# Kernel tuning notes

Hardware: AMD Instinct MI355X
Metric: run time of the kernel (lower is better)

Reference implementation:

```python
import jax, jax.numpy as jnp
import numpy as np

N_LAGS = 64
UNBIASED = False


def setup_inputs() -> dict:
    key = jax.random.key(0)
    X = jax.random.normal(key, (4096, 8192), dtype=jnp.float32)
    return {"X": X}


def reference(X) -> jnp.ndarray:
    # X: [B, T]
    B, T = X.shape
    Xc = X - jnp.mean(X, axis=1, keepdims=True)  # center per sequence
    acs = []
    for k in range(N_LAGS + 1):  # small fixed loop over lags
        denom = (T - k) if UNBIASED else T
        # sum_{t} Xc[b, t] * Xc[b, t+k]
        ac_k = jnp.einsum('bt,bt->b', Xc[:, : T - k], Xc[:, k:]) / denom
        acs.append(ac_k)
    Xautocorr = jnp.stack(acs, axis=1)  # [B, n_lags+1]
    # normalize lags 1..n_lags by lag-0 variance
    return Xautocorr[:, 1:] / Xautocorr[:, :1]
```

## Files before the change

### kernel.cpp

```cpp
#include <hip/hip_runtime.h>


typedef __bf16 bf16x8 __attribute__((ext_vector_type(8)));
typedef float f32x16 __attribute__((ext_vector_type(16)));
typedef unsigned int uint32;

#define T_LEN 8192
#define XT_STRIDE 264
#define XT_SHORTS (32 * XT_STRIDE)
#define WPB 3

__device__ __forceinline__ short f2bf(float f) {
  uint32 u = __builtin_bit_cast(uint32, f);
  return (short)((u + 0x7fffu + ((u >> 16) & 1u)) >> 16);
}

__global__ __launch_bounds__(WPB * 64, 1)
void autocorr_kernel(const float* __restrict__ X, float* __restrict__ out, int nrows) {
  __shared__ short xt_all[WPB * XT_SHORTS];
  const int wave = threadIdx.x >> 6;
  const int lane = threadIdx.x & 63;
  const int row = blockIdx.x * WPB + wave;
  if (row >= nrows) return;
  short* xt = xt_all + wave * XT_SHORTS;

  {
    int rr = lane >> 1;
    int off = 256 + ((lane & 1) << 2);
    *(int2*)(xt + rr * XT_STRIDE + off) = make_int2(0, 0);
  }

  const float4* __restrict__ Xv = (const float4*)(X + (size_t)row * T_LEN);
  float ssum = 0.f;
#pragma unroll 8
  for (int rr = 0; rr < 32; ++rr) {
    float4 v = Xv[(rr << 6) + lane];
    ssum += (v.x + v.y) + (v.z + v.w);
    int t0 = (rr << 8) + (lane << 2);
    int b = (t0 & 31) * XT_STRIDE + (t0 >> 5);
    xt[b]                 = f2bf(v.x);
    xt[b + XT_STRIDE]     = f2bf(v.y);
    xt[b + 2 * XT_STRIDE] = f2bf(v.z);
    xt[b + 3 * XT_STRIDE] = f2bf(v.w);
  }
  for (int d = 32; d > 0; d >>= 1) ssum += __shfl_xor(ssum, d, 64);

  const int r = lane & 31;
  const int hi = lane >> 5;
  f32x16 g0 = {}, g1 = {}, g2 = {};
  const short* xr = xt + r * XT_STRIDE + (hi << 3);
#pragma unroll 4
  for (int c = 0; c < 16; ++c) {
    const short* p = xr + (c << 4);
    int4 a4 = *(const int4*)p;
    int e89 = *(const int*)(p + 8);
    uint32 u0 = a4.x, u1 = a4.y, u2 = a4.z, u3 = a4.w, u4 = (uint32)e89;
    int4 b1;
    b1.x = (u0 >> 16) | (u1 << 16);
    b1.y = (u1 >> 16) | (u2 << 16);
    b1.z = (u2 >> 16) | (u3 << 16);
    b1.w = (u3 >> 16) | (u4 << 16);
    int4 b2;
    b2.x = u1; b2.y = u2; b2.z = u3; b2.w = u4;
    bf16x8 fa = __builtin_bit_cast(bf16x8, a4);
    bf16x8 f1 = __builtin_bit_cast(bf16x8, b1);
    bf16x8 f2 = __builtin_bit_cast(bf16x8, b2);
    g0 = __builtin_amdgcn_mfma_f32_32x32x16_bf16(fa, fa, g0, 0, 0, 0);
    g1 = __builtin_amdgcn_mfma_f32_32x32x16_bf16(fa, f1, g1, 0, 0, 0);
    g2 = __builtin_amdgcn_mfma_f32_32x32x16_bf16(fa, f2, g2, 0, 0, 0);
  }

  float* gbuf = (float*)xt;
#pragma unroll
  for (int v = 0; v < 16; ++v) {
    int rm = (v & 3) + (hi << 2) + ((v >> 2) << 3);
    gbuf[(rm)      * 33 + r] = g0[v];
    gbuf[(32 + rm) * 33 + r] = g1[v];
    gbuf[(64 + rm) * 33 + r] = g2[v];
  }

  int k = lane + 1;
  int s = k & 31, q = k >> 5;
  float ck = 0.f;
#pragma unroll 4
  for (int m = 0; m < 32; ++m) {
    int ms = m + s;
    int dd = q + (ms >> 5);
    ck += gbuf[(dd * 32 + m) * 33 + (ms & 31)];
  }
  float c0 = 0.f;
#pragma unroll 4
  for (int m = 0; m < 32; ++m) c0 += gbuf[m * 33 + m];

  float P = X[(size_t)row * T_LEN + lane];
  float Q = X[(size_t)row * T_LEN + (T_LEN - 1 - lane)];
  for (int d = 1; d < 64; d <<= 1) {
    float tp = __shfl_up(P, (unsigned)d, 64);
    float tq = __shfl_up(Q, (unsigned)d, 64);
    if (lane >= d) { P += tp; Q += tq; }
  }
  float mu = ssum * (1.0f / (float)T_LEN);
  float Ck = ck - mu * (2.f * ssum - P - Q) + (float)(T_LEN - k) * mu * mu;
  float C0 = c0 - mu * 2.f * ssum + (float)T_LEN * mu * mu;
  out[(size_t)row * 64 + lane] = Ck / C0;
}

extern "C" void kernel_launch(void* const* d_in, const int* in_sizes, int n_in,
                              void* d_out, int out_size, void* d_ws, size_t ws_size,
                              hipStream_t stream) {
  const float* X = (const float*)d_in[0];
  float* out = (float*)d_out;
  int nrows = in_sizes[0] / T_LEN;
  dim3 grid((nrows + WPB - 1) / WPB);
  autocorr_kernel<<<grid, dim3(WPB * 64), 0, stream>>>(X, out, nrows);
}
```

Baseline: 192.6 us.

## Feed MFMA operands directly from global loads and shrink LDS for occupancy

```diff
diff --git a/kernel.cpp b/kernel.cpp
--- a/kernel.cpp
+++ b/kernel.cpp
@@ -6,91 +6,100 @@
 typedef unsigned int uint32;
 
 #define T_LEN 8192
-#define XT_STRIDE 264
-#define XT_SHORTS (32 * XT_STRIDE)
-#define WPB 3
+#define WPB 4
+#define GB_STRIDE 34
+#define GB_SHORTS (96 * GB_STRIDE)
 
+__device__ __forceinline__ uint32 pack2bf(float a, float b) {
+  uint32 ua = __builtin_bit_cast(uint32, a);
+  uint32 ub = __builtin_bit_cast(uint32, b);
+  ua += 0x7fffu + ((ua >> 16) & 1u);
+  ub += 0x7fffu + ((ub >> 16) & 1u);
+  return (ua >> 16) | (ub & 0xffff0000u);
+}
 __device__ __forceinline__ short f2bf(float f) {
   uint32 u = __builtin_bit_cast(uint32, f);
   return (short)((u + 0x7fffu + ((u >> 16) & 1u)) >> 16);
 }
+__device__ __forceinline__ float bf2f(short h) {
+  uint32 u = ((uint32)(unsigned short)h) << 16;
+  return __builtin_bit_cast(float, u);
+}
 
-__global__ __launch_bounds__(WPB * 64, 1)
+__global__ __launch_bounds__(WPB * 64, 4)
 void autocorr_kernel(const float* __restrict__ X, float* __restrict__ out, int nrows) {
-  __shared__ short xt_all[WPB * XT_SHORTS];
+  __shared__ short gb_all[WPB * GB_SHORTS];
   const int wave = threadIdx.x >> 6;
   const int lane = threadIdx.x & 63;
   const int row = blockIdx.x * WPB + wave;
   if (row >= nrows) return;
-  short* xt = xt_all + wave * XT_SHORTS;
+  short* gb = gb_all + wave * GB_SHORTS;
 
-  {
-    int rr = lane >> 1;
-    int off = 256 + ((lane & 1) << 2);
-    *(int2*)(xt + rr * XT_STRIDE + off) = make_int2(0, 0);
+  const int m = lane & 31;
+  const int sh = lane >> 5;
+  const float* __restrict__ base = X + (size_t)row * T_LEN + (sh << 8) + m;
+
+  f32x16 g0 = {}, g1 = {}, g2 = {};
+  float ssum = 0.f;
+
+#define CHUNK_BODY(PP, E8, E9)                                                  \
+  {                                                                             \
+    float e0 = (PP)[0],   e1 = (PP)[32],  e2 = (PP)[64],  e3 = (PP)[96];        \
+    float e4 = (PP)[128], e5 = (PP)[160], e6 = (PP)[192], e7 = (PP)[224];       \
+    float e8 = (E8), e9 = (E9);                                                 \
+    ssum += ((e0 + e1) + (e2 + e3)) + ((e4 + e5) + (e6 + e7));                  \
+    uint32 u0 = pack2bf(e0, e1), u1 = pack2bf(e2, e3), u2 = pack2bf(e4, e5);    \
+    uint32 u3 = pack2bf(e6, e7), u4 = pack2bf(e8, e9);                          \
+    int4 a4 = make_int4((int)u0, (int)u1, (int)u2, (int)u3);                    \
+    int4 b1;                                                                    \
+    b1.x = (int)((u0 >> 16) | (u1 << 16));                                      \
+    b1.y = (int)((u1 >> 16) | (u2 << 16));                                      \
+    b1.z = (int)((u2 >> 16) | (u3 << 16));                                      \
+    b1.w = (int)((u3 >> 16) | (u4 << 16));                                      \
+    int4 b2 = make_int4((int)u1, (int)u2, (int)u3, (int)u4);                    \
+    bf16x8 fa = __builtin_bit_cast(bf16x8, a4);                                 \
+    bf16x8 f1 = __builtin_bit_cast(bf16x8, b1);                                 \
+    bf16x8 f2 = __builtin_bit_cast(bf16x8, b2);                                 \
+    g0 = __builtin_amdgcn_mfma_f32_32x32x16_bf16(fa, fa, g0, 0, 0, 0);          \
+    g1 = __builtin_amdgcn_mfma_f32_32x32x16_bf16(fa, f1, g1, 0, 0, 0);          \
+    g2 = __builtin_amdgcn_mfma_f32_32x32x16_bf16(fa, f2, g2, 0, 0, 0);          \
   }
 
-  const float4* __restrict__ Xv = (const float4*)(X + (size_t)row * T_LEN);
-  float ssum = 0.f;
-#pragma unroll 8
-  for (int rr = 0; rr < 32; ++rr) {
-    float4 v = Xv[(rr << 6) + lane];
-    ssum += (v.x + v.y) + (v.z + v.w);
-    int t0 = (rr << 8) + (lane << 2);
-    int b = (t0 & 31) * XT_STRIDE + (t0 >> 5);
-    xt[b]                 = f2bf(v.x);
-    xt[b + XT_STRIDE]     = f2bf(v.y);
-    xt[b + 2 * XT_STRIDE] = f2bf(v.z);
-    xt[b + 3 * XT_STRIDE] = f2bf(v.w);
+#pragma unroll 3
+  for (int c = 0; c < 15; ++c) {
+    const float* p = base + (c << 9);
+    CHUNK_BODY(p, p[256], p[288])
   }
+  {
+    const float* p = base + (15 << 9);
+    float e8s = 0.f, e9s = 0.f;
+    if (!sh) { e8s = p[256]; e9s = p[288]; }
+    CHUNK_BODY(p, e8s, e9s)
+  }
+#undef CHUNK_BODY
+
   for (int d = 32; d > 0; d >>= 1) ssum += __shfl_xor(ssum, d, 64);
 
-  const int r = lane & 31;
-  const int hi = lane >> 5;
-  f32x16 g0 = {}, g1 = {}, g2 = {};
-  const short* xr = xt + r * XT_STRIDE + (hi << 3);
-#pragma unroll 4
-  for (int c = 0; c < 16; ++c) {
-    const short* p = xr + (c << 4);
-    int4 a4 = *(const int4*)p;
-    int e89 = *(const int*)(p + 8);
-    uint32 u0 = a4.x, u1 = a4.y, u2 = a4.z, u3 = a4.w, u4 = (uint32)e89;
-    int4 b1;
-    b1.x = (u0 >> 16) | (u1 << 16);
-    b1.y = (u1 >> 16) | (u2 << 16);
-    b1.z = (u2 >> 16) | (u3 << 16);
-    b1.w = (u3 >> 16) | (u4 << 16);
-    int4 b2;
-    b2.x = u1; b2.y = u2; b2.z = u3; b2.w = u4;
-    bf16x8 fa = __builtin_bit_cast(bf16x8, a4);
-    bf16x8 f1 = __builtin_bit_cast(bf16x8, b1);
-    bf16x8 f2 = __builtin_bit_cast(bf16x8, b2);
-    g0 = __builtin_amdgcn_mfma_f32_32x32x16_bf16(fa, fa, g0, 0, 0, 0);
-    g1 = __builtin_amdgcn_mfma_f32_32x32x16_bf16(fa, f1, g1, 0, 0, 0);
-    g2 = __builtin_amdgcn_mfma_f32_32x32x16_bf16(fa, f2, g2, 0, 0, 0);
-  }
-
-  float* gbuf = (float*)xt;
 #pragma unroll
   for (int v = 0; v < 16; ++v) {
-    int rm = (v & 3) + (hi << 2) + ((v >> 2) << 3);
-    gbuf[(rm)      * 33 + r] = g0[v];
-    gbuf[(32 + rm) * 33 + r] = g1[v];
-    gbuf[(64 + rm) * 33 + r] = g2[v];
+    int rm = (v & 3) + (sh << 2) + ((v >> 2) << 3);
+    gb[(rm)      * GB_STRIDE + m] = f2bf(g0[v]);
+    gb[(32 + rm) * GB_STRIDE + m] = f2bf(g1[v]);
+    gb[(64 + rm) * GB_STRIDE + m] = f2bf(g2[v]);
   }
 
   int k = lane + 1;
-  int s = k & 31, q = k >> 5;
+  int s2 = k & 31, q = k >> 5;
   float ck = 0.f;
 #pragma unroll 4
-  for (int m = 0; m < 32; ++m) {
-    int ms = m + s;
+  for (int mm = 0; mm < 32; ++mm) {
+    int ms = mm + s2;
     int dd = q + (ms >> 5);
-    ck += gbuf[(dd * 32 + m) * 33 + (ms & 31)];
+    ck += bf2f(gb[(dd * 32 + mm) * GB_STRIDE + (ms & 31)]);
   }
   float c0 = 0.f;
 #pragma unroll 4
-  for (int m = 0; m < 32; ++m) c0 += gbuf[m * 33 + m];
+  for (int mm = 0; mm < 32; ++mm) c0 += bf2f(gb[mm * GB_STRIDE + mm]);
 
   float P = X[(size_t)row * T_LEN + lane];
   float Q = X[(size_t)row * T_LEN + (T_LEN - 1 - lane)];
```

After: 188.6 us, median of 2. 1.02x faster.
